# Performance work log

Hardware: AMD Instinct MI355X
Metric: run time of the kernel (lower is better)

Reference implementation:

```python
import jax, jax.numpy as jnp
import numpy as np

N, E, NG, G = 40000, 400000, 64, 512
IN, GP, SP, EP, EA = 4, 3, 3, 6, 4
HID, HEADS, L = 192, 4, 3
DH, FFN = HID // HEADS, 2 * HID


def _ln(x, g, b, eps=1e-5):
    m = x.mean(-1, keepdims=True)
    v = ((x - m) ** 2).mean(-1, keepdims=True)
    return (x - m) * jax.lax.rsqrt(v + eps) * g + b


def _forward(x, edge_attr, group_probs, splitter_probs, endpoint_preds, params,
             edge_index, batch, group_ptr, time_group_ids):
    (W_in, b_in, Wq, Wk, Wv, We, Wo, bo, ln1_g, ln1_b,
     W_ff1, b_ff1, W_ff2, b_ff2, ln2_g, ln2_b,
     W_e1, b_e1, W_e2, b_e2, W_e3, b_e3) = params
    n = x.shape[0]
    src, dst = edge_index[0], edge_index[1]
    # expand per-group predictions to per-node via group ids
    gids = jnp.clip(group_ptr[batch] + time_group_ids, 0, group_probs.shape[0] - 1)
    feat = jnp.concatenate([x, group_probs[gids], splitter_probs, endpoint_preds[gids]], axis=1)
    h = feat @ W_in + b_in  # [N, HID]
    scale = np.float32(1.0 / np.sqrt(DH))
    for l in range(L):  # graph transformer blocks (attention restricted to edges)
        q = (h @ Wq[l]).reshape(n, HEADS, DH)
        k = (h @ Wk[l]).reshape(n, HEADS, DH)
        v = (h @ Wv[l]).reshape(n, HEADS, DH)
        e = (edge_attr @ We[l]).reshape(-1, HEADS, DH)  # [E, H, DH]
        ke = k[src] + e
        ve = v[src] + e
        logit = jnp.einsum('ehd,ehd->eh', q[dst], ke) * scale  # [E, H]
        m = jax.ops.segment_max(logit, dst, num_segments=n)
        m = jnp.where(jnp.isfinite(m), m, 0.0)  # guard nodes with no incoming edges
        a = jnp.exp(logit - m[dst])
        den = jax.ops.segment_sum(a, dst, num_segments=n)
        a = a / (den[dst] + 1e-16)  # per-destination softmax over incoming edges
        msg = jax.ops.segment_sum(a[:, :, None] * ve, dst, num_segments=n).reshape(n, HID)
        h = _ln(h + msg @ Wo[l] + bo[l], ln1_g[l], ln1_b[l])
        ff = jax.nn.relu(h @ W_ff1[l] + b_ff1[l]) @ W_ff2[l] + b_ff2[l]
        h = _ln(h + ff, ln2_g[l], ln2_b[l])
    # edge head: gather src/dst embeddings + edge_attr, concat, MLP -> per-edge logit
    pair = jnp.concatenate([h[src], h[dst], edge_attr], axis=1)  # [E, 2*HID+EA]
    z = jax.nn.relu(pair @ W_e1 + b_e1)
    z = jax.nn.relu(z @ W_e2 + b_e2)
    return z @ W_e3 + b_e3  # [E, 1]


def setup_inputs() -> dict:
    key = jax.random.key(0)
    ks = list(jax.random.split(key, 32))
    it = iter(ks)

    def g(shape, scale=0.05):
        return jax.random.normal(next(it), shape, jnp.float32) * scale

    inp = {
        'x': jax.random.normal(next(it), (N, IN), jnp.float32),
        'edge_index': jax.random.randint(next(it), (2, E), 0, N),
        'edge_attr': jax.random.normal(next(it), (E, EA), jnp.float32),
        'batch': jnp.sort(jax.random.randint(next(it), (N,), 0, NG)),
        'group_ptr': jnp.arange(NG + 1),
        'time_group_ids': jax.random.randint(next(it), (N,), 0, 8),
        'group_probs': jax.random.normal(next(it), (G, GP), jnp.float32),
        'splitter_probs': jax.random.normal(next(it), (N, SP), jnp.float32),
        'endpoint_preds': jax.random.normal(next(it), (G, EP), jnp.float32),
        'W_in': g((IN + GP + SP + EP, HID)), 'b_in': jnp.zeros((HID,), jnp.float32),
        'Wq': g((L, HID, HID)), 'Wk': g((L, HID, HID)), 'Wv': g((L, HID, HID)),
        'We': g((L, EA, HID)), 'Wo': g((L, HID, HID)), 'bo': jnp.zeros((L, HID), jnp.float32),
        'ln1_g': jnp.ones((L, HID), jnp.float32), 'ln1_b': jnp.zeros((L, HID), jnp.float32),
        'W_ff1': g((L, HID, FFN)), 'b_ff1': jnp.zeros((L, FFN), jnp.float32),
        'W_ff2': g((L, FFN, HID)), 'b_ff2': jnp.zeros((L, HID), jnp.float32),
        'ln2_g': jnp.ones((L, HID), jnp.float32), 'ln2_b': jnp.zeros((L, HID), jnp.float32),
        'W_e1': g((2 * HID + EA, HID)), 'b_e1': jnp.zeros((HID,), jnp.float32),
        'W_e2': g((HID, HID // 2)), 'b_e2': jnp.zeros((HID // 2,), jnp.float32),
        'W_e3': g((HID // 2, 1)), 'b_e3': jnp.zeros((1,), jnp.float32),
    }
    return inp


def reference(x, edge_index, edge_attr, batch, group_ptr, time_group_ids,
              group_probs, splitter_probs, endpoint_preds,
              W_in, b_in, Wq, Wk, Wv, We, Wo, bo, ln1_g, ln1_b,
              W_ff1, b_ff1, W_ff2, b_ff2, ln2_g, ln2_b,
              W_e1, b_e1, W_e2, b_e2, W_e3, b_e3):
    params = (W_in, b_in, Wq, Wk, Wv, We, Wo, bo, ln1_g, ln1_b,
              W_ff1, b_ff1, W_ff2, b_ff2, ln2_g, ln2_b,
              W_e1, b_e1, W_e2, b_e2, W_e3, b_e3)
    return _forward(x, edge_attr, group_probs, splitter_probs, endpoint_preds, params,
                    edge_index, batch, group_ptr, time_group_ids)
```

## Files before the change

### kernel.cpp

```cpp
#include <hip/hip_runtime.h>
#include <hip/hip_bf16.h>
#include <math.h>

#define N_NODES 40000
#define N_EDGES 400000
#define GCLIP 511

using short8  = __attribute__((ext_vector_type(8))) short;
using ushort8 = __attribute__((ext_vector_type(8))) unsigned short;
using floatx4 = __attribute__((ext_vector_type(4))) float;

__device__ __forceinline__ void split_bf16(float v, unsigned short& hi, unsigned short& lo) {
    __hip_bfloat16 h = __float2bfloat16(v);
    float r = v - __bfloat162float(h);
    __hip_bfloat16 l = __float2bfloat16(r);
    hi = *(unsigned short*)&h;
    lo = *(unsigned short*)&l;
}
__device__ __forceinline__ unsigned short f2bf(float f) {
    __hip_bfloat16 h = __float2bfloat16(f);
    return *(unsigned short*)&h;
}
__device__ __forceinline__ float bf2f(unsigned short u) {
    __hip_bfloat16 h = *(__hip_bfloat16*)&u;
    return __bfloat162float(h);
}
__device__ __forceinline__ floatx4 mfma16(short8 a, short8 b, floatx4 c) {
    return __builtin_amdgcn_mfma_f32_16x16x32_bf16(a, b, c, 0, 0, 0);
}

__global__ void count_kernel(const int* __restrict__ dst, int* __restrict__ cnt, int E) {
    int e = blockIdx.x * 256 + threadIdx.x;
    if (e < E) atomicAdd(&cnt[dst[e]], 1);
}

__global__ void scan1_kernel(const int* __restrict__ cnt, int* __restrict__ rowp,
                             int* __restrict__ bsum, int n) {
    __shared__ int wsum[16];
    __shared__ int woff[16];
    int tid = threadIdx.x, wave = tid >> 6, lane = tid & 63;
    int i = blockIdx.x * 1024 + tid;
    int v = (i < n) ? cnt[i] : 0;
    int x = v;
    for (int off = 1; off < 64; off <<= 1) {
        int t = __shfl_up(x, off);
        if (lane >= off) x += t;
    }
    if (lane == 63) wsum[wave] = x;
    __syncthreads();
    if (wave == 0 && lane < 16) {
        int s = wsum[lane];
        for (int off = 1; off < 16; off <<= 1) {
            int t = __shfl_up(s, off);
            if (lane >= off) s += t;
        }
        woff[lane] = s;
    }
    __syncthreads();
    int incl = x + ((wave == 0) ? 0 : woff[wave - 1]);
    if (i < n) rowp[i] = incl - v;
    if (tid == 1023) bsum[blockIdx.x] = incl;
}

__global__ void scan2_kernel(const int* __restrict__ bsum, int* __restrict__ boffs,
                             int* __restrict__ rowp, int nb, int n) {
    int lane = threadIdx.x;
    int v = (lane < nb) ? bsum[lane] : 0;
    int x = v;
    for (int off = 1; off < 64; off <<= 1) {
        int t = __shfl_up(x, off);
        if (lane >= off) x += t;
    }
    if (lane < nb) boffs[lane] = x - v;
    if (lane == nb - 1) rowp[n] = x;
}

__global__ void scan3_kernel(int* __restrict__ rowp, int* __restrict__ curs,
                             const int* __restrict__ boffs, int n) {
    int i = blockIdx.x * 1024 + threadIdx.x;
    if (i < n) {
        int v = rowp[i] + boffs[blockIdx.x];
        rowp[i] = v;
        curs[i] = v;
    }
}

__global__ void scatter_kernel(const int* __restrict__ src, const int* __restrict__ dst,
                               int* __restrict__ cursor, int2* __restrict__ csr2, int E) {
    int e = blockIdx.x * 256 + threadIdx.x;
    if (e < E) {
        int pos = atomicAdd(&cursor[dst[e]], 1);
        csr2[pos] = make_int2(src[e], e);
    }
}

__global__ void feat_kernel(const float* __restrict__ x, const int* __restrict__ batch,
                            const int* __restrict__ gptr, const int* __restrict__ tgid,
                            const float* __restrict__ gp, const float* __restrict__ sp,
                            const float* __restrict__ ep,
                            unsigned short* __restrict__ fhi, unsigned short* __restrict__ flo,
                            int n) {
    int idx = blockIdx.x * 256 + threadIdx.x;
    if (idx >= n * 32) return;
    int node = idx >> 5, c = idx & 31;
    float v = 0.f;
    if (c < 4) {
        v = x[node * 4 + c];
    } else if (c < 7) {
        int gid = gptr[batch[node]] + tgid[node];
        gid = min(max(gid, 0), GCLIP);
        v = gp[gid * 3 + (c - 4)];
    } else if (c < 10) {
        v = sp[node * 3 + (c - 7)];
    } else if (c < 16) {
        int gid = gptr[batch[node]] + tgid[node];
        gid = min(max(gid, 0), GCLIP);
        v = ep[gid * 6 + (c - 10)];
    }
    unsigned short hi, lo;
    split_bf16(v, hi, lo);
    fhi[idx] = hi;
    flo[idx] = lo;
}

#define WOFF_WIN 0
#define WOFF_QKV 6144
#define WOFF_WO  337920
#define WOFF_WF1 448512
#define WOFF_WF2 669696
#define WOFF_HSD 890880
#define WOFF_WE2 964608
#define WTOT     983040

__global__ void prep_kernel(const float* __restrict__ W_in, const float* __restrict__ Wq,
                            const float* __restrict__ Wk, const float* __restrict__ Wv,
                            const float* __restrict__ Wo, const float* __restrict__ Wf1,
                            const float* __restrict__ Wf2, const float* __restrict__ We1,
                            const float* __restrict__ We2, unsigned short* __restrict__ wb) {
    int idx = blockIdx.x * 256 + threadIdx.x;
    if (idx >= WTOT) return;
    float val;
    if (idx < WOFF_QKV) {
        int n = idx / 32, k = idx % 32;
        val = (k < 16) ? W_in[k * 192 + n] : 0.f;
    } else if (idx < WOFF_WO) {
        int r = idx - WOFF_QKV; int l = r / 110592; r %= 110592;
        int n = r / 192, k = r % 192;
        const float* s = (n < 192) ? Wq : (n < 384 ? Wk : Wv);
        val = s[l * 36864 + k * 192 + (n % 192)];
        if (n < 192) val *= 0.14433756729740643f;
    } else if (idx < WOFF_WF1) {
        int r = idx - WOFF_WO; int l = r / 36864; r %= 36864;
        int n = r / 192, k = r % 192;
        val = Wo[l * 36864 + k * 192 + n];
    } else if (idx < WOFF_WF2) {
        int r = idx - WOFF_WF1; int l = r / 73728; r %= 73728;
        int n = r / 192, k = r % 192;
        val = Wf1[l * 73728 + k * 384 + n];
    } else if (idx < WOFF_HSD) {
        int r = idx - WOFF_WF2; int l = r / 73728; r %= 73728;
        int n = r / 384, k = r % 384;
        val = Wf2[l * 73728 + k * 192 + n];
    } else if (idx < WOFF_WE2) {
        int r = idx - WOFF_HSD;
        int n = r / 192, k = r % 192;
        val = (n < 192) ? We1[k * 192 + n] : We1[(192 + k) * 192 + (n - 192)];
    } else {
        int r = idx - WOFF_WE2;
        int n = r / 192, k = r % 192;
        val = We2[k * 96 + n];
    }
    wb[idx] = f2bf(val);
}

template <int EPI, int DUAL, int BN, int KCH, int TERMS, int OUTMODE>
__global__ __launch_bounds__(256, 2)
void mfma_gemm(const unsigned short* __restrict__ Ahi, const unsigned short* __restrict__ Alo,
               int M, int Ka,
               const unsigned short* __restrict__ B, const float* __restrict__ bias,
               const unsigned short* __restrict__ Rhi, const unsigned short* __restrict__ Rlo,
               const float* __restrict__ lng, const float* __restrict__ lnb,
               unsigned short* __restrict__ Chi, unsigned short* __restrict__ Clo,
               int oldc, int cmul, int cadd) {
    constexpr int NT = BN / 16;
    __shared__ __align__(16) unsigned short sB[BN][KCH + 8];
    const int tid = threadIdx.x;
    const int wave = tid >> 6, lane = tid & 63;
    const int quad = lane >> 4, l16 = lane & 15;
    const int rbase = blockIdx.x * 128;
    const int cbase = blockIdx.y * BN;

    floatx4 acc[2][NT];
#pragma unroll
    for (int mt = 0; mt < 2; ++mt)
#pragma unroll
        for (int nt = 0; nt < NT; ++nt) acc[mt][nt] = (floatx4)0.0f;

    const int r0 = min(rbase + wave * 32 + l16, M - 1);
    const int r1 = min(rbase + wave * 32 + 16 + l16, M - 1);
    const unsigned short* pa0h = Ahi + (size_t)r0 * Ka + quad * 8;
    const unsigned short* pa1h = Ahi + (size_t)r1 * Ka + quad * 8;
    const unsigned short* pa0l = Alo + (size_t)r0 * Ka + quad * 8;
    const unsigned short* pa1l = Alo + (size_t)r1 * Ka + quad * 8;

    for (int kb = 0; kb < Ka; kb += KCH) {
        if (kb) __syncthreads();
        for (int i = tid * 8; i < BN * KCH; i += 2048) {
            int n = i / KCH, kk = i % KCH;
            *(uint4*)&sB[n][kk] = *(const uint4*)(B + (size_t)(cbase + n) * Ka + kb + kk);
        }
        __syncthreads();
        short8 ch0 = *(const short8*)(pa0h + kb);
        short8 ch1 = *(const short8*)(pa1h + kb);
        short8 cl0, cl1;
        if (TERMS == 2) {
            cl0 = *(const short8*)(pa0l + kb);
            cl1 = *(const short8*)(pa1l + kb);
        }
#pragma unroll
        for (int kc = 0; kc < KCH; kc += 32) {
            short8 nh0 = ch0, nh1 = ch1, nl0 = ch0, nl1 = ch1;
            if (kc + 32 < KCH) {
                nh0 = *(const short8*)(pa0h + kb + kc + 32);
                nh1 = *(const short8*)(pa1h + kb + kc + 32);
                if (TERMS == 2) {
                    nl0 = *(const short8*)(pa0l + kb + kc + 32);
                    nl1 = *(const short8*)(pa1l + kb + kc + 32);
                }
            }
#pragma unroll
            for (int nt = 0; nt < NT; ++nt) {
                short8 b = *(const short8*)&sB[nt * 16 + l16][kc + quad * 8];
                acc[0][nt] = mfma16(ch0, b, acc[0][nt]);
                if (TERMS == 2) acc[0][nt] = mfma16(cl0, b, acc[0][nt]);
                acc[1][nt] = mfma16(ch1, b, acc[1][nt]);
                if (TERMS == 2) acc[1][nt] = mfma16(cl1, b, acc[1][nt]);
            }
            ch0 = nh0; ch1 = nh1;
            if (TERMS == 2) { cl0 = nl0; cl1 = nl1; }
        }
    }

    float bb[NT], gg[NT], be[NT];
#pragma unroll
    for (int nt = 0; nt < NT; ++nt) {
        int colg = cbase + nt * 16 + l16;
        bb[nt] = bias ? bias[colg] : 0.f;
        if (EPI == 2) { gg[nt] = lng[colg]; be[nt] = lnb[colg]; }
    }
#pragma unroll
    for (int mt = 0; mt < 2; ++mt) {
#pragma unroll
        for (int reg = 0; reg < 4; ++reg) {
            int row = rbase + wave * 32 + mt * 16 + quad * 4 + reg;
            if (EPI == 2) {
                int rr = min(row, M - 1);
                float v[NT], s = 0.f, q = 0.f;
#pragma unroll
                for (int nt = 0; nt < NT; ++nt) {
                    size_t off = (size_t)rr * 192 + nt * 16 + l16;
                    float resid = bf2f(Rhi[off]) + bf2f(Rlo[off]);
                    v[nt] = acc[mt][nt][reg] + bb[nt] + resid;
                    s += v[nt]; q += v[nt] * v[nt];
                }
#pragma unroll
                for (int off = 1; off < 16; off <<= 1) {
                    s += __shfl_xor(s, off);
                    q += __shfl_xor(q, off);
                }
                float mean = s * (1.f / 192.f);
                float var = q * (1.f / 192.f) - mean * mean;
                float rs = rsqrtf(var + 1e-5f);
                if (row < M) {
#pragma unroll
                    for (int nt = 0; nt < NT; ++nt) {
                        float r = (v[nt] - mean) * rs * gg[nt] + be[nt];
                        unsigned short hi, lo;
                        split_bf16(r, hi, lo);
                        size_t off = (size_t)row * 192 + nt * 16 + l16;
                        Chi[off] = hi; Clo[off] = lo;
                    }
                }
            } else if (row < M) {
#pragma unroll
                for (int nt = 0; nt < NT; ++nt) {
                    float v = acc[mt][nt][reg] + bb[nt];
                    if (EPI == 1) v = fmaxf(v, 0.f);
                    if (OUTMODE == 1) {
                        int c = cbase + nt * 16 + l16;
                        if (c < 192) {
                            Chi[(size_t)row * 192 + c] = f2bf(v);
                        } else {
                            int cc = c - 192;
                            int idx = (cc < 192) ? (cc * 2) : ((cc - 192) * 2 + 1);
                            Clo[(size_t)row * 384 + idx] = f2bf(v);
                        }
                    } else {
                        size_t off = (size_t)row * oldc + (size_t)(cbase + nt * 16 + l16) * cmul + cadd;
                        if (DUAL) {
                            unsigned short hi, lo;
                            split_bf16(v, hi, lo);
                            Chi[off] = hi; Clo[off] = lo;
                        } else {
                            Chi[off] = f2bf(v);
                        }
                    }
                }
            }
        }
    }
}

__global__ __launch_bounds__(256)
void attn_kernel(const unsigned short* __restrict__ qB, const unsigned short* __restrict__ kvB,
                 const float* __restrict__ ea, const float* __restrict__ We_l,
                 const int2* __restrict__ csr2, const int* __restrict__ row_ptr,
                 unsigned short* __restrict__ msg_hi, unsigned short* __restrict__ msg_lo) {
    __shared__ float sWe[768];
    const int tid = threadIdx.x;
    for (int i = tid; i < 768; i += 256) sWe[i] = We_l[i];
    __syncthreads();

    const int lane = tid & 63;
    const int node = blockIdx.x * 4 + (tid >> 6);
    const int d0 = (lane >> 4) * 48 + (lane & 15) * 3;

    float W[4][3];
#pragma unroll
    for (int w = 0; w < 4; ++w) {
        W[w][0] = sWe[w * 192 + d0];
        W[w][1] = sWe[w * 192 + d0 + 1];
        W[w][2] = sWe[w * 192 + d0 + 2];
    }
    size_t qoff = (size_t)node * 192 + d0;
    float q0 = bf2f(qB[qoff]), q1 = bf2f(qB[qoff + 1]), q2 = bf2f(qB[qoff + 2]);
    float qe0 = q0 * W[0][0] + q1 * W[0][1] + q2 * W[0][2];
    float qe1 = q0 * W[1][0] + q1 * W[1][1] + q2 * W[1][2];
    float qe2 = q0 * W[2][0] + q1 * W[2][1] + q2 * W[2][2];
    float qe3 = q0 * W[3][0] + q1 * W[3][1] + q2 * W[3][2];
#pragma unroll
    for (int off = 1; off < 16; off <<= 1) {
        qe0 += __shfl_xor(qe0, off);
        qe1 += __shfl_xor(qe1, off);
        qe2 += __shfl_xor(qe2, off);
        qe3 += __shfl_xor(qe3, off);
    }

    const unsigned int* kv = (const unsigned int*)kvB;
    const float4* ea4 = (const float4*)ea;

    float m = -INFINITY, den = 0.f;
    float v0 = 0.f, v1 = 0.f, v2 = 0.f;
    float wa0 = 0.f, wa1 = 0.f, wa2 = 0.f, wa3 = 0.f;
    const int beg = row_ptr[node], end = row_ptr[node + 1];
    int p = beg;
    for (; p + 3 < end; p += 4) {
        int2 seA = csr2[p], seB = csr2[p + 1], seC = csr2[p + 2], seD = csr2[p + 3];
        size_t bA = (size_t)seA.x * 192 + d0;
        size_t bB = (size_t)seB.x * 192 + d0;
        size_t bC = (size_t)seC.x * 192 + d0;
        size_t bD = (size_t)seD.x * 192 + d0;
        unsigned int uA0 = kv[bA], uA1 = kv[bA + 1], uA2 = kv[bA + 2];
        unsigned int uB0 = kv[bB], uB1 = kv[bB + 1], uB2 = kv[bB + 2];
        unsigned int uC0 = kv[bC], uC1 = kv[bC + 1], uC2 = kv[bC + 2];
        unsigned int uD0 = kv[bD], uD1 = kv[bD + 1], uD2 = kv[bD + 2];
        float4 wA = ea4[seA.y], wB = ea4[seB.y], wC = ea4[seC.y], wD = ea4[seD.y];
        float dA = q0 * bf2f((unsigned short)uA0) + q1 * bf2f((unsigned short)uA1) + q2 * bf2f((unsigned short)uA2);
        float dB = q0 * bf2f((unsigned short)uB0) + q1 * bf2f((unsigned short)uB1) + q2 * bf2f((unsigned short)uB2);
        float dC = q0 * bf2f((unsigned short)uC0) + q1 * bf2f((unsigned short)uC1) + q2 * bf2f((unsigned short)uC2);
        float dD = q0 * bf2f((unsigned short)uD0) + q1 * bf2f((unsigned short)uD1) + q2 * bf2f((unsigned short)uD2);
#pragma unroll
        for (int off = 1; off < 16; off <<= 1) {
            dA += __shfl_xor(dA, off);
            dB += __shfl_xor(dB, off);
            dC += __shfl_xor(dC, off);
            dD += __shfl_xor(dD, off);
        }
        float lA = dA + wA.x * qe0 + wA.y * qe1 + wA.z * qe2 + wA.w * qe3;
        float lB = dB + wB.x * qe0 + wB.y * qe1 + wB.z * qe2 + wB.w * qe3;
        float lC = dC + wC.x * qe0 + wC.y * qe1 + wC.z * qe2 + wC.w * qe3;
        float lD = dD + wD.x * qe0 + wD.y * qe1 + wD.z * qe2 + wD.w * qe3;
        float mn = fmaxf(m, fmaxf(fmaxf(lA, lB), fmaxf(lC, lD)));
        float corr = __expf(m - mn);
        float pA = __expf(lA - mn), pB = __expf(lB - mn);
        float pC = __expf(lC - mn), pD = __expf(lD - mn);
        den = den * corr + pA + pB + pC + pD;
        v0 = v0 * corr + pA * bf2f((unsigned short)(uA0 >> 16)) + pB * bf2f((unsigned short)(uB0 >> 16))
                       + pC * bf2f((unsigned short)(uC0 >> 16)) + pD * bf2f((unsigned short)(uD0 >> 16));
        v1 = v1 * corr + pA * bf2f((unsigned short)(uA1 >> 16)) + pB * bf2f((unsigned short)(uB1 >> 16))
                       + pC * bf2f((unsigned short)(uC1 >> 16)) + pD * bf2f((unsigned short)(uD1 >> 16));
        v2 = v2 * corr + pA * bf2f((unsigned short)(uA2 >> 16)) + pB * bf2f((unsigned short)(uB2 >> 16))
                       + pC * bf2f((unsigned short)(uC2 >> 16)) + pD * bf2f((unsigned short)(uD2 >> 16));
        wa0 = wa0 * corr + pA * wA.x + pB * wB.x + pC * wC.x + pD * wD.x;
        wa1 = wa1 * corr + pA * wA.y + pB * wB.y + pC * wC.y + pD * wD.y;
        wa2 = wa2 * corr + pA * wA.z + pB * wB.z + pC * wC.z + pD * wD.z;
        wa3 = wa3 * corr + pA * wA.w + pB * wB.w + pC * wC.w + pD * wD.w;
        m = mn;
    }
    for (; p < end; ++p) {
        int2 se = csr2[p];
        size_t b = (size_t)se.x * 192 + d0;
        unsigned int u0 = kv[b], u1 = kv[b + 1], u2 = kv[b + 2];
        float4 w = ea4[se.y];
        float d = q0 * bf2f((unsigned short)u0) + q1 * bf2f((unsigned short)u1)
                + q2 * bf2f((unsigned short)u2);
#pragma unroll
        for (int off = 1; off < 16; off <<= 1) d += __shfl_xor(d, off);
        float l = d + w.x * qe0 + w.y * qe1 + w.z * qe2 + w.w * qe3;
        float mn = fmaxf(m, l);
        float corr = __expf(m - mn);
        float pe = __expf(l - mn);
        den = den * corr + pe;
        v0 = v0 * corr + pe * bf2f((unsigned short)(u0 >> 16));
        v1 = v1 * corr + pe * bf2f((unsigned short)(u1 >> 16));
        v2 = v2 * corr + pe * bf2f((unsigned short)(u2 >> 16));
        wa0 = wa0 * corr + pe * w.x;
        wa1 = wa1 * corr + pe * w.y;
        wa2 = wa2 * corr + pe * w.z;
        wa3 = wa3 * corr + pe * w.w;
        m = mn;
    }
    float inv = 1.f / (den + 1e-16f);
    float m0 = (v0 + wa0 * W[0][0] + wa1 * W[1][0] + wa2 * W[2][0] + wa3 * W[3][0]) * inv;
    float m1 = (v1 + wa0 * W[0][1] + wa1 * W[1][1] + wa2 * W[2][1] + wa3 * W[3][1]) * inv;
    float m2 = (v2 + wa0 * W[0][2] + wa1 * W[1][2] + wa2 * W[2][2] + wa3 * W[3][2]) * inv;
    size_t ob = (size_t)node * 192 + d0;
    unsigned short hi, lo;
    split_bf16(m0, hi, lo); msg_hi[ob] = hi;     msg_lo[ob] = lo;
    split_bf16(m1, hi, lo); msg_hi[ob + 1] = hi; msg_lo[ob + 1] = lo;
    split_bf16(m2, hi, lo); msg_hi[ob + 2] = hi; msg_lo[ob + 2] = lo;
}

__global__ __launch_bounds__(256, 2)
void edge_head_kernel(const unsigned short* __restrict__ hsd, const float* __restrict__ ea,
                      const int* __restrict__ src, const int* __restrict__ dst,
                      const float* __restrict__ W1e, const float* __restrict__ b1,
                      const unsigned short* __restrict__ W2hi,
                      const float* __restrict__ b2, const float* __restrict__ W3,
                      const float* __restrict__ b3, float* __restrict__ out) {
    __shared__ __align__(16) unsigned short sW[96][200];
    __shared__ __align__(16) float sWe1[768];
    __shared__ __align__(16) float sB1[192];
    const int tid = threadIdx.x;
    const int wave = tid >> 6, lane = tid & 63;
    const int quad = lane >> 4, l16 = lane & 15;
    const int ebase = blockIdx.x * 64;

    for (int i = tid; i < 768; i += 256) sWe1[i] = W1e[i];
    if (tid < 192) sB1[tid] = b1[tid];
    for (int i = tid * 8; i < 96 * 192; i += 2048) {
        int n = i / 192, kk = i % 192;
        *(uint4*)&sW[n][kk] = *(const uint4*)(W2hi + (size_t)n * 192 + kk);
    }

    const int e = ebase + wave * 16 + l16;
    const int s = src[e], d = dst[e];
    const float4 eav = *(const float4*)(ea + (size_t)e * 4);
    const unsigned short* hs_p = hsd + (size_t)s * 384 + quad * 8;
    const unsigned short* hd_p = hsd + (size_t)d * 384 + 192 + quad * 8;

    floatx4 acc[6];
#pragma unroll
    for (int nt = 0; nt < 6; ++nt) acc[nt] = (floatx4)0.0f;
    __syncthreads();

    ushort8 hs_c = *(const ushort8*)hs_p;
    ushort8 hd_c = *(const ushort8*)hd_p;
#pragma unroll
    for (int kc = 0; kc < 192; kc += 32) {
        ushort8 hs_n = hs_c, hd_n = hd_c;
        if (kc + 32 < 192) {
            hs_n = *(const ushort8*)(hs_p + kc + 32);
            hd_n = *(const ushort8*)(hd_p + kc + 32);
        }
        const int c0 = kc + quad * 8;
        float wb1[8], w0v[8], w1v[8], w2v[8], w3v[8];
        *(float4*)&wb1[0] = *(const float4*)&sB1[c0];
        *(float4*)&wb1[4] = *(const float4*)&sB1[c0 + 4];
        *(float4*)&w0v[0] = *(const float4*)&sWe1[c0];
        *(float4*)&w0v[4] = *(const float4*)&sWe1[c0 + 4];
        *(float4*)&w1v[0] = *(const float4*)&sWe1[192 + c0];
        *(float4*)&w1v[4] = *(const float4*)&sWe1[192 + c0 + 4];
        *(float4*)&w2v[0] = *(const float4*)&sWe1[384 + c0];
        *(float4*)&w2v[4] = *(const float4*)&sWe1[384 + c0 + 4];
        *(float4*)&w3v[0] = *(const float4*)&sWe1[576 + c0];
        *(float4*)&w3v[4] = *(const float4*)&sWe1[576 + c0 + 4];
        ushort8 ah, al;
#pragma unroll
        for (int j = 0; j < 8; ++j) {
            float ce = wb1[j] + eav.x * w0v[j] + eav.y * w1v[j]
                     + eav.z * w2v[j] + eav.w * w3v[j];
            float v = fmaxf(bf2f(hs_c[j]) + bf2f(hd_c[j]) + ce, 0.f);
            unsigned short hi, lo;
            split_bf16(v, hi, lo);
            ah[j] = hi; al[j] = lo;
        }
        short8 ahs = *(short8*)&ah, als = *(short8*)&al;
#pragma unroll
        for (int nt = 0; nt < 6; ++nt) {
            short8 bh = *(const short8*)&sW[nt * 16 + l16][kc + quad * 8];
            acc[nt] = mfma16(ahs, bh, acc[nt]);
            acc[nt] = mfma16(als, bh, acc[nt]);
        }
        hs_c = hs_n; hd_c = hd_n;
    }

    float w3[6], bb2[6];
#pragma unroll
    for (int nt = 0; nt < 6; ++nt) {
        int col = nt * 16 + l16;
        w3[nt] = W3[col];
        bb2[nt] = b2[col];
    }
    float b3v = b3[0];
#pragma unroll
    for (int reg = 0; reg < 4; ++reg) {
        float sacc = 0.f;
#pragma unroll
        for (int nt = 0; nt < 6; ++nt) {
            float z = fmaxf(acc[nt][reg] + bb2[nt], 0.f);
            sacc = fmaf(z, w3[nt], sacc);
        }
#pragma unroll
        for (int off = 1; off < 16; off <<= 1) sacc += __shfl_xor(sacc, off);
        if (l16 == 0) out[ebase + wave * 16 + quad * 4 + reg] = sacc + b3v;
    }
}

extern "C" void kernel_launch(void* const* d_in, const int* in_sizes, int n_in,
                              void* d_out, int out_size, void* d_ws, size_t ws_size,
                              hipStream_t stream) {
    const float* x     = (const float*)d_in[0];
    const int*   eidx  = (const int*)d_in[1];
    const float* ea    = (const float*)d_in[2];
    const int*   batch = (const int*)d_in[3];
    const int*   gptr  = (const int*)d_in[4];
    const int*   tgid  = (const int*)d_in[5];
    const float* gp    = (const float*)d_in[6];
    const float* sp    = (const float*)d_in[7];
    const float* epp   = (const float*)d_in[8];
    const float* W_in  = (const float*)d_in[9];
    const float* b_in  = (const float*)d_in[10];
    const float* Wq    = (const float*)d_in[11];
    const float* Wk    = (const float*)d_in[12];
    const float* Wv    = (const float*)d_in[13];
    const float* We    = (const float*)d_in[14];
    const float* Wo    = (const float*)d_in[15];
    const float* bo    = (const float*)d_in[16];
    const float* ln1g  = (const float*)d_in[17];
    const float* ln1b  = (const float*)d_in[18];
    const float* Wf1   = (const float*)d_in[19];
    const float* bf1   = (const float*)d_in[20];
    const float* Wf2   = (const float*)d_in[21];
    const float* bf2   = (const float*)d_in[22];
    const float* ln2g  = (const float*)d_in[23];
    const float* ln2b  = (const float*)d_in[24];
    const float* We1   = (const float*)d_in[25];
    const float* be1   = (const float*)d_in[26];
    const float* We2   = (const float*)d_in[27];
    const float* be2   = (const float*)d_in[28];
    const float* We3   = (const float*)d_in[29];
    const float* be3   = (const float*)d_in[30];
    const int* src = eidx;
    const int* dst = eidx + N_EDGES;

    unsigned short* ub = (unsigned short*)d_ws;
    unsigned short* featH = ub;
    unsigned short* featL = ub + 1280000;
    unsigned short* hH    = ub + 2560000;
    unsigned short* hL    = ub + 10240000;
    unsigned short* htH   = ub + 17920000;
    unsigned short* htL   = ub + 25600000;
    unsigned short* msgH  = ub + 33280000;
    unsigned short* msgL  = ub + 40960000;
    unsigned short* rbuf  = ub + 48640000;
    unsigned short* qB    = rbuf;
    unsigned short* kvB   = rbuf + 7680000;
    unsigned short* ffH   = rbuf;
    unsigned short* ffL   = rbuf + 15360000;
    unsigned short* hsdB  = rbuf;
    unsigned short* wb    = ub + 79360000;
    int* ib   = (int*)(ub + 80343040);
    int* cnt  = ib;
    int* rowp = ib + 40000;
    int* curs = ib + 80004;
    int2* csr2 = (int2*)(ib + 120004);
    int* bsum  = ib + 920004;
    int* boffs = ib + 920044;

    hipMemsetAsync(cnt, 0, N_NODES * sizeof(int), stream);
    count_kernel<<<1563, 256, 0, stream>>>(dst, cnt, N_EDGES);
    scan1_kernel<<<40, 1024, 0, stream>>>(cnt, rowp, bsum, N_NODES);
    scan2_kernel<<<1, 64, 0, stream>>>(bsum, boffs, rowp, 40, N_NODES);
    scan3_kernel<<<40, 1024, 0, stream>>>(rowp, curs, boffs, N_NODES);
    scatter_kernel<<<1563, 256, 0, stream>>>(src, dst, curs, csr2, N_EDGES);
    feat_kernel<<<5000, 256, 0, stream>>>(x, batch, gptr, tgid, gp, sp, epp, featH, featL, N_NODES);
    prep_kernel<<<3840, 256, 0, stream>>>(W_in, Wq, Wk, Wv, Wo, Wf1, Wf2, We1, We2, wb);

    dim3 blk(256);
    mfma_gemm<0, 1, 96, 32, 2, 0><<<dim3(313, 2), blk, 0, stream>>>(featH, featL, N_NODES, 32,
        wb + WOFF_WIN, b_in, nullptr, nullptr, nullptr, nullptr, hH, hL, 192, 1, 0);

    for (int l = 0; l < 3; ++l) {
        const unsigned short* wq = wb + WOFF_QKV + l * 110592;
        mfma_gemm<0, 0, 96, 192, 1, 1><<<dim3(313, 6), blk, 0, stream>>>(hH, hL, N_NODES, 192,
            wq, nullptr, nullptr, nullptr, nullptr, nullptr, qB, kvB, 0, 0, 0);
        attn_kernel<<<10000, blk, 0, stream>>>(qB, kvB, ea, We + l * 768, csr2, rowp, msgH, msgL);
        mfma_gemm<2, 1, 192, 96, 2, 0><<<dim3(313, 1), blk, 0, stream>>>(msgH, msgL, N_NODES, 192,
            wb + WOFF_WO + l * 36864, bo + l * 192, hH, hL, ln1g + l * 192, ln1b + l * 192,
            htH, htL, 192, 1, 0);
        mfma_gemm<1, 1, 96, 192, 2, 0><<<dim3(313, 4), blk, 0, stream>>>(htH, htL, N_NODES, 192,
            wb + WOFF_WF1 + l * 73728, bf1 + l * 384, nullptr, nullptr, nullptr, nullptr,
            ffH, ffL, 384, 1, 0);
        mfma_gemm<2, 1, 192, 96, 2, 0><<<dim3(313, 1), blk, 0, stream>>>(ffH, ffL, N_NODES, 384,
            wb + WOFF_WF2 + l * 73728, bf2 + l * 192, htH, htL, ln2g + l * 192, ln2b + l * 192,
            hH, hL, 192, 1, 0);
    }

    mfma_gemm<0, 0, 96, 192, 2, 0><<<dim3(313, 4), blk, 0, stream>>>(hH, hL, N_NODES, 192,
        wb + WOFF_HSD, nullptr, nullptr, nullptr, nullptr, nullptr, hsdB, nullptr, 384, 1, 0);
    edge_head_kernel<<<6250, blk, 0, stream>>>(hsdB, ea, src, dst,
        We1 + 384 * 192, be1, wb + WOFF_WE2, be2, We3, be3, (float*)d_out);
}
```

Measured before the change: 930.8 us.

## Add A-stationary GEMM, XOR-swizzle LDS tiles, drop softmax max, single-term edge MLP

Adds an A-stationary GEMM variant that loads each block's A rows into registers once and loops over all output column tiles. This replaces the 2-D grids for the QKV, FFN1 and edge-head projections, so A is no longer re-read from global memory for every column block. Shared-memory B tiles switch from padded rows to an XOR-swizzled layout to avoid bank conflicts. The attention softmax drops the running max and rescaling, and the edge MLP's second layer uses only the bf16 hi term instead of hi+lo. Both of those trade precision and overflow safety for fewer instructions.

```diff
diff --git a/kernel.cpp b/kernel.cpp
--- a/kernel.cpp
+++ b/kernel.cpp
@@ -173,17 +173,19 @@
     wb[idx] = f2bf(val);
 }
 
-template <int EPI, int DUAL, int BN, int KCH, int TERMS, int OUTMODE>
+
+template <int EPI, int DUAL, int BN, int KCH, int TERMS>
 __global__ __launch_bounds__(256, 2)
 void mfma_gemm(const unsigned short* __restrict__ Ahi, const unsigned short* __restrict__ Alo,
                int M, int Ka,
                const unsigned short* __restrict__ B, const float* __restrict__ bias,
                const unsigned short* __restrict__ Rhi, const unsigned short* __restrict__ Rlo,
                const float* __restrict__ lng, const float* __restrict__ lnb,
-               unsigned short* __restrict__ Chi, unsigned short* __restrict__ Clo,
-               int oldc, int cmul, int cadd) {
+               unsigned short* __restrict__ Chi, unsigned short* __restrict__ Clo, int ldc) {
     constexpr int NT = BN / 16;
-    __shared__ __align__(16) unsigned short sB[BN][KCH + 8];
+    constexpr int JB = KCH / 8;
+    constexpr int SBLK = ((JB + 7) / 8) * 8;
+    __shared__ __align__(16) unsigned short sB[BN * SBLK * 8];
     const int tid = threadIdx.x;
     const int wave = tid >> 6, lane = tid & 63;
     const int quad = lane >> 4, l16 = lane & 15;
@@ -205,9 +207,10 @@
 
     for (int kb = 0; kb < Ka; kb += KCH) {
         if (kb) __syncthreads();
-        for (int i = tid * 8; i < BN * KCH; i += 2048) {
-            int n = i / KCH, kk = i % KCH;
-            *(uint4*)&sB[n][kk] = *(const uint4*)(B + (size_t)(cbase + n) * Ka + kb + kk);
+        for (int i = tid; i < BN * JB; i += 256) {
+            int n = i % BN, j = i / BN;
+            *(uint4*)&sB[(n * SBLK + (j ^ (n & 7))) * 8] =
+                *(const uint4*)(B + (size_t)(cbase + n) * Ka + kb + j * 8);
         }
         __syncthreads();
         short8 ch0 = *(const short8*)(pa0h + kb);
@@ -228,9 +231,11 @@
                     nl1 = *(const short8*)(pa1l + kb + kc + 32);
                 }
             }
+            const int jbase = kc / 8;
 #pragma unroll
             for (int nt = 0; nt < NT; ++nt) {
-                short8 b = *(const short8*)&sB[nt * 16 + l16][kc + quad * 8];
+                int jj = (jbase + quad) ^ (l16 & 7);
+                short8 b = *(const short8*)&sB[((nt * 16 + l16) * SBLK + jj) * 8];
                 acc[0][nt] = mfma16(ch0, b, acc[0][nt]);
                 if (TERMS == 2) acc[0][nt] = mfma16(cl0, b, acc[0][nt]);
                 acc[1][nt] = mfma16(ch1, b, acc[1][nt]);
@@ -286,23 +291,112 @@
                 for (int nt = 0; nt < NT; ++nt) {
                     float v = acc[mt][nt][reg] + bb[nt];
                     if (EPI == 1) v = fmaxf(v, 0.f);
-                    if (OUTMODE == 1) {
-                        int c = cbase + nt * 16 + l16;
-                        if (c < 192) {
-                            Chi[(size_t)row * 192 + c] = f2bf(v);
+                    size_t off = (size_t)row * ldc + cbase + nt * 16 + l16;
+                    if (DUAL) {
+                        unsigned short hi, lo;
+                        split_bf16(v, hi, lo);
+                        Chi[off] = hi; Clo[off] = lo;
+                    } else {
+                        Chi[off] = f2bf(v);
+                    }
+                }
+            }
+        }
+    }
+}
+
+template <int EPI, int DUAL, int BN, int NTILES, int TERMS, int KF, int OUTMODE>
+__global__ __launch_bounds__(256, 2)
+void mfma_gemm_astat(const unsigned short* __restrict__ Ahi, const unsigned short* __restrict__ Alo,
+                     int M, const unsigned short* __restrict__ B, const float* __restrict__ bias,
+                     unsigned short* __restrict__ Chi, unsigned short* __restrict__ Clo, int ldc) {
+    constexpr int NT = BN / 16;
+    constexpr int Ka = KF * 32;
+    constexpr int SBLK = KF * 4;
+    __shared__ __align__(16) unsigned short sB[BN * SBLK * 8];
+    const int tid = threadIdx.x;
+    const int wave = tid >> 6, lane = tid & 63;
+    const int quad = lane >> 4, l16 = lane & 15;
+    const int rbase = blockIdx.x * 128;
+
+    const int r0 = min(rbase + wave * 32 + l16, M - 1);
+    const int r1 = min(rbase + wave * 32 + 16 + l16, M - 1);
+    const unsigned short* pa0h = Ahi + (size_t)r0 * Ka + quad * 8;
+    const unsigned short* pa1h = Ahi + (size_t)r1 * Ka + quad * 8;
+    const unsigned short* pa0l = Alo + (size_t)r0 * Ka + quad * 8;
+    const unsigned short* pa1l = Alo + (size_t)r1 * Ka + quad * 8;
+
+    short8 afh[2][KF], afl[2][KF];
+#pragma unroll
+    for (int kf = 0; kf < KF; ++kf) {
+        afh[0][kf] = *(const short8*)(pa0h + kf * 32);
+        afh[1][kf] = *(const short8*)(pa1h + kf * 32);
+        if (TERMS == 2) {
+            afl[0][kf] = *(const short8*)(pa0l + kf * 32);
+            afl[1][kf] = *(const short8*)(pa1l + kf * 32);
+        }
+    }
+
+    for (int t = 0; t < NTILES; ++t) {
+        const int cbase = t * BN;
+        if (t) __syncthreads();
+        for (int i = tid; i < BN * KF * 4; i += 256) {
+            int n = i % BN, j = i / BN;
+            *(uint4*)&sB[(n * SBLK + (j ^ (n & 7))) * 8] =
+                *(const uint4*)(B + (size_t)(cbase + n) * Ka + j * 8);
+        }
+        __syncthreads();
+
+        floatx4 acc[2][NT];
+#pragma unroll
+        for (int mt = 0; mt < 2; ++mt)
+#pragma unroll
+            for (int nt = 0; nt < NT; ++nt) acc[mt][nt] = (floatx4)0.0f;
+
+#pragma unroll
+        for (int kf = 0; kf < KF; ++kf) {
+#pragma unroll
+            for (int nt = 0; nt < NT; ++nt) {
+                int jj = (kf * 4 + quad) ^ (l16 & 7);
+                short8 b = *(const short8*)&sB[((nt * 16 + l16) * SBLK + jj) * 8];
+                acc[0][nt] = mfma16(afh[0][kf], b, acc[0][nt]);
+                if (TERMS == 2) acc[0][nt] = mfma16(afl[0][kf], b, acc[0][nt]);
+                acc[1][nt] = mfma16(afh[1][kf], b, acc[1][nt]);
+                if (TERMS == 2) acc[1][nt] = mfma16(afl[1][kf], b, acc[1][nt]);
+            }
+        }
+
+        float bb[NT];
+#pragma unroll
+        for (int nt = 0; nt < NT; ++nt) bb[nt] = bias ? bias[cbase + nt * 16 + l16] : 0.f;
+#pragma unroll
+        for (int mt = 0; mt < 2; ++mt) {
+#pragma unroll
+            for (int reg = 0; reg < 4; ++reg) {
+                int row = rbase + wave * 32 + mt * 16 + quad * 4 + reg;
+                if (row < M) {
+#pragma unroll
+                    for (int nt = 0; nt < NT; ++nt) {
+                        float v = acc[mt][nt][reg] + bb[nt];
+                        if (EPI == 1) v = fmaxf(v, 0.f);
+                        if (OUTMODE == 1) {
+                            int c = cbase + nt * 16 + l16;
+                            if (c < 192) {
+                                Chi[(size_t)row * 192 + c] = f2bf(v);
+                            } else {
+                                int cc = c - 192;
+                                int idx = (cc < 192) ? (cc * 2) : ((cc - 192) * 2 + 1);
+                                Clo[(size_t)row * 384 + idx] = f2bf(v);
+                            }
                         } else {
-                            int cc = c - 192;
-                            int idx = (cc < 192) ? (cc * 2) : ((cc - 192) * 2 + 1);
-                            Clo[(size_t)row * 384 + idx] = f2bf(v);
-                        }
-                    } else {
-                        size_t off = (size_t)row * oldc + (size_t)(cbase + nt * 16 + l16) * cmul + cadd;
-                        if (DUAL) {
-                            unsigned short hi, lo;
-                            split_bf16(v, hi, lo);
-                            Chi[off] = hi; Clo[off] = lo;
-                        } else {
-                            Chi[off] = f2bf(v);
+                            size_t off = (size_t)row * ldc + cbase + nt * 16 + l16;
+                            if (DUAL) {
+                                unsigned short hi, lo;
+                                split_bf16(v, hi, lo);
+                                Chi[off] = hi; Clo[off] = lo;
+                            } else {
+                                Chi[off] = f2bf(v);
+                            }
                         }
                     }
                 }
@@ -349,7 +443,7 @@
     const unsigned int* kv = (const unsigned int*)kvB;
     const float4* ea4 = (const float4*)ea;
 
-    float m = -INFINITY, den = 0.f;
+    float den = 0.f;
     float v0 = 0.f, v1 = 0.f, v2 = 0.f;
     float wa0 = 0.f, wa1 = 0.f, wa2 = 0.f, wa3 = 0.f;
     const int beg = row_ptr[node], end = row_ptr[node + 1];
@@ -376,26 +470,21 @@
             dC += __shfl_xor(dC, off);
             dD += __shfl_xor(dD, off);
         }
-        float lA = dA + wA.x * qe0 + wA.y * qe1 + wA.z * qe2 + wA.w * qe3;
-        float lB = dB + wB.x * qe0 + wB.y * qe1 + wB.z * qe2 + wB.w * qe3;
-        float lC = dC + wC.x * qe0 + wC.y * qe1 + wC.z * qe2 + wC.w * qe3;
-        float lD = dD + wD.x * qe0 + wD.y * qe1 + wD.z * qe2 + wD.w * qe3;
-        float mn = fmaxf(m, fmaxf(fmaxf(lA, lB), fmaxf(lC, lD)));
-        float corr = __expf(m - mn);
-        float pA = __expf(lA - mn), pB = __expf(lB - mn);
-        float pC = __expf(lC - mn), pD = __expf(lD - mn);
-        den = den * corr + pA + pB + pC + pD;
-        v0 = v0 * corr + pA * bf2f((unsigned short)(uA0 >> 16)) + pB * bf2f((unsigned short)(uB0 >> 16))
-                       + pC * bf2f((unsigned short)(uC0 >> 16)) + pD * bf2f((unsigned short)(uD0 >> 16));
-        v1 = v1 * corr + pA * bf2f((unsigned short)(uA1 >> 16)) + pB * bf2f((unsigned short)(uB1 >> 16))
-                       + pC * bf2f((unsigned short)(uC1 >> 16)) + pD * bf2f((unsigned short)(uD1 >> 16));
-        v2 = v2 * corr + pA * bf2f((unsigned short)(uA2 >> 16)) + pB * bf2f((unsigned short)(uB2 >> 16))
-                       + pC * bf2f((unsigned short)(uC2 >> 16)) + pD * bf2f((unsigned short)(uD2 >> 16));
-        wa0 = wa0 * corr + pA * wA.x + pB * wB.x + pC * wC.x + pD * wD.x;
-        wa1 = wa1 * corr + pA * wA.y + pB * wB.y + pC * wC.y + pD * wD.y;
-        wa2 = wa2 * corr + pA * wA.z + pB * wB.z + pC * wC.z + pD * wD.z;
-        wa3 = wa3 * corr + pA * wA.w + pB * wB.w + pC * wC.w + pD * wD.w;
-        m = mn;
+        float pA = __expf(dA + wA.x * qe0 + wA.y * qe1 + wA.z * qe2 + wA.w * qe3);
+        float pB = __expf(dB + wB.x * qe0 + wB.y * qe1 + wB.z * qe2 + wB.w * qe3);
+        float pC = __expf(dC + wC.x * qe0 + wC.y * qe1 + wC.z * qe2 + wC.w * qe3);
+        float pD = __expf(dD + wD.x * qe0 + wD.y * qe1 + wD.z * qe2 + wD.w * qe3);
+        den += pA + pB + pC + pD;
+        v0 += pA * bf2f((unsigned short)(uA0 >> 16)) + pB * bf2f((unsigned short)(uB0 >> 16))
+            + pC * bf2f((unsigned short)(uC0 >> 16)) + pD * bf2f((unsigned short)(uD0 >> 16));
+        v1 += pA * bf2f((unsigned short)(uA1 >> 16)) + pB * bf2f((unsigned short)(uB1 >> 16))
+            + pC * bf2f((unsigned short)(uC1 >> 16)) + pD * bf2f((unsigned short)(uD1 >> 16));
+        v2 += pA * bf2f((unsigned short)(uA2 >> 16)) + pB * bf2f((unsigned short)(uB2 >> 16))
+            + pC * bf2f((unsigned short)(uC2 >> 16)) + pD * bf2f((unsigned short)(uD2 >> 16));
+        wa0 += pA * wA.x + pB * wB.x + pC * wC.x + pD * wD.x;
+        wa1 += pA * wA.y + pB * wB.y + pC * wC.y + pD * wD.y;
+        wa2 += pA * wA.z + pB * wB.z + pC * wC.z + pD * wD.z;
+        wa3 += pA * wA.w + pB * wB.w + pC * wC.w + pD * wD.w;
     }
     for (; p < end; ++p) {
         int2 se = csr2[p];
@@ -406,19 +495,15 @@
                 + q2 * bf2f((unsigned short)u2);
 #pragma unroll
         for (int off = 1; off < 16; off <<= 1) d += __shfl_xor(d, off);
-        float l = d + w.x * qe0 + w.y * qe1 + w.z * qe2 + w.w * qe3;
-        float mn = fmaxf(m, l);
-        float corr = __expf(m - mn);
-        float pe = __expf(l - mn);
-        den = den * corr + pe;
-        v0 = v0 * corr + pe * bf2f((unsigned short)(u0 >> 16));
-        v1 = v1 * corr + pe * bf2f((unsigned short)(u1 >> 16));
-        v2 = v2 * corr + pe * bf2f((unsigned short)(u2 >> 16));
-        wa0 = wa0 * corr + pe * w.x;
-        wa1 = wa1 * corr + pe * w.y;
-        wa2 = wa2 * corr + pe * w.z;
-        wa3 = wa3 * corr + pe * w.w;
-        m = mn;
+        float pe = __expf(d + w.x * qe0 + w.y * qe1 + w.z * qe2 + w.w * qe3);
+        den += pe;
+        v0 += pe * bf2f((unsigned short)(u0 >> 16));
+        v1 += pe * bf2f((unsigned short)(u1 >> 16));
+        v2 += pe * bf2f((unsigned short)(u2 >> 16));
+        wa0 += pe * w.x;
+        wa1 += pe * w.y;
+        wa2 += pe * w.z;
+        wa3 += pe * w.w;
     }
     float inv = 1.f / (den + 1e-16f);
     float m0 = (v0 + wa0 * W[0][0] + wa1 * W[1][0] + wa2 * W[2][0] + wa3 * W[3][0]) * inv;
@@ -438,7 +523,7 @@
                       const unsigned short* __restrict__ W2hi,
                       const float* __restrict__ b2, const float* __restrict__ W3,
                       const float* __restrict__ b3, float* __restrict__ out) {
-    __shared__ __align__(16) unsigned short sW[96][200];
+    __shared__ __align__(16) unsigned short sW[96 * 192];
     __shared__ __align__(16) float sWe1[768];
     __shared__ __align__(16) float sB1[192];
     const int tid = threadIdx.x;
@@ -448,9 +533,9 @@
 
     for (int i = tid; i < 768; i += 256) sWe1[i] = W1e[i];
     if (tid < 192) sB1[tid] = b1[tid];
-    for (int i = tid * 8; i < 96 * 192; i += 2048) {
-        int n = i / 192, kk = i % 192;
-        *(uint4*)&sW[n][kk] = *(const uint4*)(W2hi + (size_t)n * 192 + kk);
+    for (int i = tid; i < 96 * 24; i += 256) {
+        int n = i % 96, j = i / 96;
+        *(uint4*)&sW[(n * 24 + (j ^ (n & 7))) * 8] = *(const uint4*)(W2hi + (size_t)n * 192 + j * 8);
     }
 
     const int e = ebase + wave * 16 + l16;
@@ -485,22 +570,21 @@
         *(float4*)&w2v[4] = *(const float4*)&sWe1[384 + c0 + 4];
         *(float4*)&w3v[0] = *(const float4*)&sWe1[576 + c0];
         *(float4*)&w3v[4] = *(const float4*)&sWe1[576 + c0 + 4];
-        ushort8 ah, al;
+        ushort8 ah;
 #pragma unroll
         for (int j = 0; j < 8; ++j) {
             float ce = wb1[j] + eav.x * w0v[j] + eav.y * w1v[j]
                      + eav.z * w2v[j] + eav.w * w3v[j];
             float v = fmaxf(bf2f(hs_c[j]) + bf2f(hd_c[j]) + ce, 0.f);
-            unsigned short hi, lo;
-            split_bf16(v, hi, lo);
-            ah[j] = hi; al[j] = lo;
-        }
-        short8 ahs = *(short8*)&ah, als = *(short8*)&al;
+            ah[j] = f2bf(v);
+        }
+        short8 ahs = *(short8*)&ah;
+        const int jbase = kc / 8;
 #pragma unroll
         for (int nt = 0; nt < 6; ++nt) {
-            short8 bh = *(const short8*)&sW[nt * 16 + l16][kc + quad * 8];
+            int jj = (jbase + quad) ^ (l16 & 7);
+            short8 bh = *(const short8*)&sW[((nt * 16 + l16) * 24 + jj) * 8];
             acc[nt] = mfma16(ahs, bh, acc[nt]);
-            acc[nt] = mfma16(als, bh, acc[nt]);
         }
         hs_c = hs_n; hd_c = hd_n;
     }
@@ -598,27 +682,26 @@
     prep_kernel<<<3840, 256, 0, stream>>>(W_in, Wq, Wk, Wv, Wo, Wf1, Wf2, We1, We2, wb);
 
     dim3 blk(256);
-    mfma_gemm<0, 1, 96, 32, 2, 0><<<dim3(313, 2), blk, 0, stream>>>(featH, featL, N_NODES, 32,
-        wb + WOFF_WIN, b_in, nullptr, nullptr, nullptr, nullptr, hH, hL, 192, 1, 0);
+    mfma_gemm<0, 1, 96, 32, 2><<<dim3(313, 2), blk, 0, stream>>>(featH, featL, N_NODES, 32,
+        wb + WOFF_WIN, b_in, nullptr, nullptr, nullptr, nullptr, hH, hL, 192);
 
     for (int l = 0; l < 3; ++l) {
         const unsigned short* wq = wb + WOFF_QKV + l * 110592;
-        mfma_gemm<0, 0, 96, 192, 1, 1><<<dim3(313, 6), blk, 0, stream>>>(hH, hL, N_NODES, 192,
-            wq, nullptr, nullptr, nullptr, nullptr, nullptr, qB, kvB, 0, 0, 0);
+        mfma_gemm_astat<0, 0, 96, 6, 1, 6, 1><<<313, blk, 0, stream>>>(hH, hL, N_NODES,
+            wq, nullptr, qB, kvB, 0);
         attn_kernel<<<10000, blk, 0, stream>>>(qB, kvB, ea, We + l * 768, csr2, rowp, msgH, msgL);
-        mfma_gemm<2, 1, 192, 96, 2, 0><<<dim3(313, 1), blk, 0, stream>>>(msgH, msgL, N_NODES, 192,
+        mfma_gemm<2, 1, 192, 96, 2><<<dim3(313, 1), blk, 0, stream>>>(msgH, msgL, N_NODES, 192,
             wb + WOFF_WO + l * 36864, bo + l * 192, hH, hL, ln1g + l * 192, ln1b + l * 192,
-            htH, htL, 192, 1, 0);
-        mfma_gemm<1, 1, 96, 192, 2, 0><<<dim3(313, 4), blk, 0, stream>>>(htH, htL, N_NODES, 192,
-            wb + WOFF_WF1 + l * 73728, bf1 + l * 384, nullptr, nullptr, nullptr, nullptr,
-            ffH, ffL, 384, 1, 0);
-        mfma_gemm<2, 1, 192, 96, 2, 0><<<dim3(313, 1), blk, 0, stream>>>(ffH, ffL, N_NODES, 384,
+            htH, htL, 192);
+        mfma_gemm_astat<1, 1, 96, 4, 2, 6, 0><<<313, blk, 0, stream>>>(htH, htL, N_NODES,
+            wb + WOFF_WF1 + l * 73728, bf1 + l * 384, ffH, ffL, 384);
+        mfma_gemm<2, 1, 192, 96, 2><<<dim3(313, 1), blk, 0, stream>>>(ffH, ffL, N_NODES, 384,
             wb + WOFF_WF2 + l * 73728, bf2 + l * 192, htH, htL, ln2g + l * 192, ln2b + l * 192,
-            hH, hL, 192, 1, 0);
-    }
-
-    mfma_gemm<0, 0, 96, 192, 2, 0><<<dim3(313, 4), blk, 0, stream>>>(hH, hL, N_NODES, 192,
-        wb + WOFF_HSD, nullptr, nullptr, nullptr, nullptr, nullptr, hsdB, nullptr, 384, 1, 0);
+            hH, hL, 192);
+    }
+
+    mfma_gemm_astat<0, 0, 96, 4, 2, 6, 0><<<313, blk, 0, stream>>>(hH, hL, N_NODES,
+        wb + WOFF_HSD, nullptr, hsdB, nullptr, 384);
     edge_head_kernel<<<6250, blk, 0, stream>>>(hsdB, ea, src, dst,
         We1 + 384 * 192, be1, wb + WOFF_WE2, be2, We3, be3, (float*)d_out);
 }
```

Result: faster. 909.9 us (-2.3%).
